# Kernel tuning notes

Hardware: AMD Instinct MI355X
Metric: run time of the kernel (lower is better)

The kernel has to match this reference:

```python
import jax, jax.numpy as jnp
import numpy as np

B, NH, N = 4, 4, 1000
NF = 256
TOPK = 10
ADJ_THRESH = 0.5
PSTEP = 3
BIG = 1e10


def construct_edges(s_cur, a_cur):
    """Top-k distance-based edge construction.
    s_cur: (B,N,3) positions, a_cur: (B,N) attributes; tool = a_cur > 0.5.
    Returns dense receiver/sender matrices Rr, Rs of shape (B, R=N*TOPK, N),
    padded with zero rows (equivalent to torch's contiguous packing).
    """
    b, n, _ = s_cur.shape
    tool = a_cur > 0.5  # mask is all-ones (no particle_nums)
    diff = s_cur[:, :, None, :] - s_cur[:, None, :, :]          # (B,N,N,3)
    dis = jnp.sum(diff * diff, axis=-1)                          # (B,N,N)
    # tool-tool pairs excluded (set huge distance)
    dis = jnp.where(tool[:, :, None] & tool[:, None, :], BIG, dis)
    neg_d, idx = jax.lax.top_k(-dis, TOPK)                       # smallest TOPK dists
    d = -neg_d                                                    # (B,N,TOPK)
    # edge valid if within threshold; receiver-is-tool edges zeroed
    # (connect_tools_all=False branch: adj[tool_mask_1 * mask_2] = 0)
    flag = (d < ADJ_THRESH * ADJ_THRESH) & (~tool[:, :, None])   # (B,N,TOPK)
    R = n * TOPK
    flagR = flag.reshape(b, R).astype(s_cur.dtype)
    send = idx.reshape(b, R)                                      # sender index per relation
    recv = jnp.repeat(jnp.arange(n), TOPK)                        # (R,) receiver index
    bi = jnp.arange(b)[:, None]
    ri = jnp.arange(R)[None, :]
    Rr = jnp.zeros((b, R, n), s_cur.dtype).at[bi, ri, recv[None, :]].set(flagR)
    Rs = jnp.zeros((b, R, n), s_cur.dtype).at[bi, ri, send].set(flagR)
    return Rr, Rs


def _forward(a_hist, s_hist, s_delta,
             pe_w0, pe_b0, pe_w1, pe_b1,
             re_w0, re_b0, re_w1, re_b1, re_w2, re_b2,
             rp_w, rp_b, pp_w, pp_b,
             pr_w0, pr_b0, pr_w1, pr_b1):
    relu = jax.nn.relu
    b, nh, n = a_hist.shape
    a = jnp.swapaxes(a_hist, 1, 2)                 # (B,N,NH)
    s = jnp.swapaxes(s_hist, 1, 2)                 # (B,N,NH,3)
    sd = jnp.swapaxes(s_delta, 1, 2).reshape(b, n, 3 * nh)  # (B,N,3*NH)
    a_cur = a[:, :, -1]                             # (B,N)
    s_cur = s[:, :, -1, :]                          # (B,N,3)

    Rr, Rs = construct_edges(s_cur, a_cur)          # (B,R,N)

    a_r = jnp.einsum('brn,bn->br', Rr, a_cur)[..., None]  # (B,R,1)
    a_s = jnp.einsum('brn,bn->br', Rs, a_cur)[..., None]
    s_r = jnp.einsum('brn,bnd->brd', Rr, s_cur)            # (B,R,3)
    s_s = jnp.einsum('brn,bnd->brd', Rs, s_cur)

    # particle encoder: Linear-ReLU-Linear-ReLU on cat[s_delta_flat, a_hist]
    pe_in = jnp.concatenate([sd, a], axis=2)               # (B,N,4*NH)
    particle_encode = relu(relu(pe_in @ pe_w0 + pe_b0) @ pe_w1 + pe_b1)

    re_in = jnp.concatenate([a_r, a_s, s_r - s_s], axis=2)
    h = relu(re_in @ re_w0 + re_b0)
    h = relu(h @ re_w1 + re_b1)
    relation_encode = relu(h @ re_w2 + re_b2)              # (B,R,NF)

    particle_effect = particle_encode
    for _ in range(PSTEP):
        eff_r = jnp.einsum('brn,bnd->brd', Rr, particle_effect)
        eff_s = jnp.einsum('brn,bnd->brd', Rs, particle_effect)
        effect_rel = relu(
            jnp.concatenate([relation_encode, eff_r, eff_s], axis=2) @ rp_w + rp_b)
        agg = jnp.einsum('brn,brd->bnd', Rr, effect_rel)   # Rr^T @ effect_rel
        particle_effect = relu(
            jnp.concatenate([particle_encode, agg], axis=2) @ pp_w + pp_b
            + particle_effect)

    pred = relu(particle_effect @ pr_w0 + pr_b0) @ pr_w1 + pr_b1  # (B,N,3)
    return pred + s_cur


def setup_inputs() -> dict:
    key = jax.random.key(0)
    ks = jax.random.split(key, 24)
    W = lambda k, shp: (jax.random.normal(k, shp, jnp.float32) * 0.05)
    inp = {
        'a_hist': jax.random.uniform(ks[0], (B, NH, N), jnp.float32),
        's_hist': jax.random.normal(ks[1], (B, NH, N, 3), jnp.float32),
        's_delta': jax.random.normal(ks[2], (B, NH, N, 3), jnp.float32),
        'pe_w0': W(ks[3], (4 * NH, NF)), 'pe_b0': W(ks[4], (NF,)),
        'pe_w1': W(ks[5], (NF, NF)),     'pe_b1': W(ks[6], (NF,)),
        're_w0': W(ks[7], (5, NF)),      're_b0': W(ks[8], (NF,)),
        're_w1': W(ks[9], (NF, NF)),     're_b1': W(ks[10], (NF,)),
        're_w2': W(ks[11], (NF, NF)),    're_b2': W(ks[12], (NF,)),
        'rp_w': W(ks[13], (3 * NF, NF)), 'rp_b': W(ks[14], (NF,)),
        'pp_w': W(ks[15], (2 * NF, NF)), 'pp_b': W(ks[16], (NF,)),
        'pr_w0': W(ks[17], (NF, NF)),    'pr_b0': W(ks[18], (NF,)),
        'pr_w1': W(ks[19], (NF, 3)),     'pr_b1': W(ks[20], (3,)),
    }
    return inp


def reference(a_hist, s_hist, s_delta,
              pe_w0, pe_b0, pe_w1, pe_b1,
              re_w0, re_b0, re_w1, re_b1, re_w2, re_b2,
              rp_w, rp_b, pp_w, pp_b,
              pr_w0, pr_b0, pr_w1, pr_b1):
    return _forward(a_hist, s_hist, s_delta,
                    pe_w0, pe_b0, pe_w1, pe_b1,
                    re_w0, re_b0, re_w1, re_b1, re_w2, re_b2,
                    rp_w, rp_b, pp_w, pp_b,
                    pr_w0, pr_b0, pr_w1, pr_b1)
```

## Files before the change

kernel.cpp:

```cpp
#include <hip/hip_runtime.h>
#include <hip/hip_bf16.h>

typedef unsigned short u16;
typedef unsigned int u32;

#define BATCH 4
#define NHIST 4
#define NPART 1000
#define NTOPK 10
#define NPT (BATCH*NPART)
#define NET (NPT*NTOPK)
#define EREG 5000
#define NRT 157

typedef __bf16 b8v __attribute__((ext_vector_type(8)));
typedef float  f4v __attribute__((ext_vector_type(4)));

__device__ __forceinline__ float bf2f(u16 b){
    return __uint_as_float(((u32)b) << 16);
}
__device__ __forceinline__ u16 f2bf(float f){
    u32 u = __float_as_uint(f);
    u32 r = u + 0x7FFF + ((u >> 16) & 1);
    return (u16)(r >> 16);
}
__device__ __forceinline__ float ldin(const void* p, size_t i, int isf32){
    return isf32 ? ((const float*)p)[i] : bf2f(((const u16*)p)[i]);
}
__device__ __forceinline__ void unp8(uint4 v, float* d){
    d[0]=bf2f((u16)v.x); d[1]=bf2f((u16)(v.x>>16));
    d[2]=bf2f((u16)v.y); d[3]=bf2f((u16)(v.y>>16));
    d[4]=bf2f((u16)v.z); d[5]=bf2f((u16)(v.z>>16));
    d[6]=bf2f((u16)v.w); d[7]=bf2f((u16)(v.w>>16));
}
__device__ __forceinline__ u32 pk2(float a, float b){
    return (u32)f2bf(a) | ((u32)f2bf(b) << 16);
}

__global__ __launch_bounds__(256) void k_setup(
    const void* __restrict__ a_hist, const void* __restrict__ s_hist,
    const void* __restrict__ s_delta,
    const void* w0, const void* w1, const void* w2, const void* w3,
    const void* w4, const void* w5, const void* w6, const void* w7,
    u16* __restrict__ wsw, int* __restrict__ dflag,
    float* __restrict__ s_cur, u16* __restrict__ pe_in,
    int* __restrict__ ecount8, int* __restrict__ cidx, int* __restrict__ csend,
    u16* __restrict__ re_in)
{
    __shared__ u32 SMEM[8192];
    __shared__ int sdet;
    __shared__ int wcnt[4], wbase[4];
    int t = threadIdx.x;
    if (t == 0) sdet = 0;
    __syncthreads();
    {
        const u16* p = (const u16*)a_hist;
        int bad = 0;
        for (int i = t; i < 2000; i += 256) bad |= (p[i] >> 15) & 1;
        if (bad) atomicOr(&sdet, 1);
    }
    __syncthreads();
    int isf32 = sdet;
    int bid = blockIdx.x;

    if (bid < 74){
        const int nck[8] = {1,8,1,8,8,24,16,8};
        const int Ks[8]  = {16,256,5,256,256,768,512,256};
        const void* srcs[8] = {w0,w1,w2,w3,w4,w5,w6,w7};
        int wi = 0, c = bid;
        while (c >= nck[wi]){ c -= nck[wi]; wi++; }
        const void* src = srcs[wi];
        int K = Ks[wi];
        u16* stage = (u16*)SMEM;
        #pragma unroll 4
        for (int kk = 0; kk < 32; kk++){
            int k = c*32 + kk;
            float v = (k < K) ? ldin(src, (size_t)k*256 + t, isf32) : 0.f;
            int e = (t >> 4)*512 + ((kk >> 3)*16 + (t & 15))*8 + (kk & 7);
            stage[e] = f2bf(v);
        }
        __syncthreads();
        uint4* dstv = (uint4*)(wsw + (size_t)bid * 8192);
        const uint4* sv = (const uint4*)stage;
        dstv[t] = sv[t];
        dstv[t + 256] = sv[t + 256];
        dstv[t + 512] = sv[t + 512];
        dstv[t + 768] = sv[t + 768];
        return;
    }
    if (bid < 90){
        if (bid == 74 && t == 0) dflag[0] = isf32;
        int g = (bid - 74)*256 + t;
        if (g >= NPT) return;
        int b = g / NPART, i = g - b*NPART;
        #pragma unroll
        for (int d = 0; d < 3; d++)
            s_cur[g*3 + d] = ldin(s_hist, (size_t)((b*NHIST + NHIST-1)*NPART + i)*3 + d, isf32);
        #pragma unroll
        for (int h = 0; h < NHIST; h++){
            #pragma unroll
            for (int d = 0; d < 3; d++)
                pe_in[g*32 + h*3 + d] = f2bf(ldin(s_delta, (size_t)((b*NHIST + h)*NPART + i)*3 + d, isf32));
            pe_in[g*32 + 12 + h] = f2bf(ldin(a_hist, (b*NHIST + h)*NPART + i, isf32));
        }
        #pragma unroll
        for (int k = 16; k < 32; k++) pe_in[g*32 + k] = 0;
        return;
    }
    float* sx = (float*)SMEM;
    float* sy = sx + 1000;
    float* sz = sx + 2000;
    float* sa = sx + 3000;
    u32* raw  = SMEM + 4096;
    u32* rawa = SMEM + 4096 + 3072;
    int tb = bid - 90;
    int b = tb / 250, r0 = (tb % 250) * 4;
    int wid = t >> 6, lane = t & 63;
    {
        int sbase = (b*NHIST + NHIST-1)*NPART*3;
        int abase = (b*NHIST + NHIST-1)*NPART;
        if (isf32){
            const uint4* ps = (const uint4*)((const float*)s_hist + sbase);
            for (int i = t; i < 750; i += 256) ((uint4*)raw)[i] = ps[i];
            const uint4* pa = (const uint4*)((const float*)a_hist + abase);
            if (t < 250) ((uint4*)rawa)[t] = pa[t];
        } else {
            const uint4* ps = (const uint4*)((const u16*)s_hist + sbase);
            for (int i = t; i < 375; i += 256) ((uint4*)raw)[i] = ps[i];
            const uint4* pa = (const uint4*)((const u16*)a_hist + abase);
            if (t < 125) ((uint4*)rawa)[t] = pa[t];
        }
    }
    __syncthreads();
    for (int j = t; j < NPART; j += 256){
        float vx, vy, vz, va;
        if (isf32){
            vx = ((const float*)raw)[j*3+0]; vy = ((const float*)raw)[j*3+1];
            vz = ((const float*)raw)[j*3+2]; va = ((const float*)rawa)[j];
        } else {
            vx = bf2f(((const u16*)raw)[j*3+0]); vy = bf2f(((const u16*)raw)[j*3+1]);
            vz = bf2f(((const u16*)raw)[j*3+2]); va = bf2f(((const u16*)rawa)[j]);
        }
        sx[j] = vx; sy[j] = vy; sz[j] = vz; sa[j] = va;
    }
    __syncthreads();
    int i = r0 + wid;
    float xi = sx[i], yi = sy[i], zi = sz[i];
    float ai = sa[i];
    bool tool_i = ai > 0.5f;
    float thr = tool_i ? -1.0f : 0.25f;

    float bd[NTOPK]; int bj[NTOPK];
    #pragma unroll
    for (int k = 0; k < NTOPK; k++){ bd[k] = 3.0e38f; bj[k] = 1 << 30; }
    for (int j = lane; j < NPART; j += 64){
        float dx = xi - sx[j], dy = yi - sy[j], dz = zi - sz[j];
        float d = dx*dx + dy*dy + dz*dz;
        if (d < thr && d < bd[NTOPK-1]){
            float v = d; int vj = j;
            #pragma unroll
            for (int k = 0; k < NTOPK; k++){
                bool sw = v < bd[k];
                float tv = bd[k]; int tj = bj[k];
                if (sw){ bd[k] = v; bj[k] = vj; v = tv; vj = tj; }
            }
        }
    }
    float myd = 3.0e38f; int myj = 0;
    #pragma unroll
    for (int r = 0; r < NTOPK; r++){
        float v = bd[0]; int vj = bj[0];
        #pragma unroll
        for (int s = 32; s > 0; s >>= 1){
            float ov = __shfl_xor(v, s);
            int   oj = __shfl_xor(vj, s);
            if (ov < v || (ov == v && oj < vj)){ v = ov; vj = oj; }
        }
        if (lane == r){ myd = v; myj = vj; }
        bool owner = (bd[0] == v) && (bj[0] == vj);
        if (owner){
            #pragma unroll
            for (int k = 0; k < NTOPK-1; k++){ bd[k] = bd[k+1]; bj[k] = bj[k+1]; }
            bd[NTOPK-1] = 3.0e38f; bj[NTOPK-1] = 1 << 30;
        }
    }
    bool fl = (lane < NTOPK) && (myd < 0.25f);
    int cnt = __popcll(__ballot(fl));
    if (lane == 0) wcnt[wid] = cnt;
    __syncthreads();
    if (t == 0){
        int c0 = wcnt[0], c1 = wcnt[1], c2 = wcnt[2], c3 = wcnt[3];
        int reg = tb & 7;
        int bb = atomicAdd(&ecount8[reg], c0 + c1 + c2 + c3) + reg*EREG;
        wbase[0] = bb; wbase[1] = bb + c0; wbase[2] = bb + c0 + c1; wbase[3] = bb + c0 + c1 + c2;
    }
    __syncthreads();
    int base = wbase[wid];
    if (lane < NTOPK){
        int gp = b*NPART + i;
        int ce = fl ? base + lane : -1;
        cidx[gp*NTOPK + lane] = ce;
        if (ce >= 0){
            int j = myj;
            csend[ce] = b*NPART + j;
            u32 q0 = (u32)f2bf(ai)        | ((u32)f2bf(sa[j])      << 16);
            u32 q1 = (u32)f2bf(xi - sx[j]) | ((u32)f2bf(yi - sy[j]) << 16);
            u32 q2 = (u32)f2bf(zi - sz[j]);
            uint4 v0 = {q0, q1, q2, 0};
            uint4 zz = {0, 0, 0, 0};
            uint4* rp = (uint4*)(re_in + (size_t)ce*32);
            rp[0] = v0; rp[1] = zz; rp[2] = zz; rp[3] = zz;
        }
    }
}

__global__ __launch_bounds__(256) void k_edge(
    const u16* __restrict__ re_in, const u16* __restrict__ pe_in,
    const u16* __restrict__ W0, const u16* __restrict__ W1,
    const u16* __restrict__ W2, const u16* __restrict__ W3,
    const u16* __restrict__ PW0, const u16* __restrict__ PW1,
    const u16* __restrict__ WrpB,
    const void* __restrict__ B0, const void* __restrict__ B1,
    const void* __restrict__ B2,
    const void* __restrict__ PB0, const void* __restrict__ PB1,
    const int* __restrict__ dflag, const int* __restrict__ ecount8,
    u16* __restrict__ Eout, u16* __restrict__ penc,
    u16* __restrict__ Pr, u16* __restrict__ Ps)
{
    __shared__ u16 H1[32*256];
    __shared__ u16 H2[32*256];
    __shared__ u16 S[32*32];
    int t = threadIdx.x, lane = t & 63, wave = t >> 6;
    int wm = wave >> 1, wn = wave & 1;
    int isf32 = dflag[0];
    int l15 = lane & 15, l4 = lane >> 4;

    f4v acc[8];
    b8v af, bfA[8], bfB[8];
    auto zacc = [&](){
        #pragma unroll
        for (int j = 0; j < 8; j++) acc[j] = {0.f,0.f,0.f,0.f};
    };
    auto rdWto = [&](b8v* dst, const u16* W, int kc){
        #pragma unroll
        for (int j = 0; j < 8; j++)
            dst[j] = *(const b8v*)(W + (size_t)kc*8192 + ((wn*8 + j)*64 + lane)*8);
    };
    auto domf = [&](b8v* wf){
        #pragma unroll
        for (int j = 0; j < 8; j++)
            acc[j] = __builtin_amdgcn_mfma_f32_16x16x32_bf16(af, wf[j], acc[j], 0, 0, 0);
    };
    auto rdA = [&](const u16* Hin, int kc){
        int R = wm*16 + l15;
        int up = (kc*4 + l4) ^ (R & 31);
        af = *(const b8v*)&Hin[R*256 + up*8];
    };
    auto layer = [&](const u16* Hin, const u16* Wg){
        zacc();
        rdWto(bfA, Wg, 0);
        #pragma unroll
        for (int kc = 0; kc < 8; kc += 2){
            rdWto(bfB, Wg, kc + 1);
            rdA(Hin, kc); domf(bfA);
            if (kc + 2 < 8) rdWto(bfA, Wg, kc + 2);
            rdA(Hin, kc + 1); domf(bfB);
        }
    };
    auto epiLDS = [&](u16* Hout, const void* Wb){
        #pragma unroll
        for (int j = 0; j < 8; j++){
            int col = (wn*8 + j)*16 + l15;
            float bias = ldin(Wb, col, isf32);
            int rb = wm*16 + l4*4;
            #pragma unroll
            for (int r = 0; r < 4; r++){
                float v = acc[j][r] + bias;
                v = v > 0.f ? v : 0.f;
                int rr = rb + r;
                int up = (col >> 3) ^ (rr & 31);
                Hout[rr*256 + up*8 + (col & 7)] = f2bf(v);
            }
        }
    };
    auto stLin = [&](u16* C, int row0){
        #pragma unroll
        for (int j = 0; j < 8; j++){
            int col = (wn*8 + j)*16 + l15;
            int rb = row0 + wm*16 + l4*4;
            #pragma unroll
            for (int r = 0; r < 4; r++)
                C[(size_t)(rb + r)*256 + col] = f2bf(acc[j][r]);
        }
    };

    if (blockIdx.x >= 8*NRT){
        int row0 = (blockIdx.x - 8*NRT) * 32;
        if (t < 128){
            int row = t >> 2, q = t & 3;
            int rg = row0 + row;
            uint4 v = *(const uint4*)(pe_in + (size_t)rg*32 + q*8);
            int up = q ^ (row & 3);
            *(uint4*)&S[row*32 + up*8] = v;
        }
        __syncthreads();
        zacc();
        {
            rdWto(bfA, PW0, 0);
            int R = wm*16 + l15;
            int up = l4 ^ (R & 3);
            af = *(const b8v*)&S[R*32 + up*8];
            domf(bfA);
        }
        epiLDS(H1, PB0);
        __syncthreads();
        layer(H1, PW1);
        #pragma unroll
        for (int j = 0; j < 8; j++){
            int col = (wn*8 + j)*16 + l15;
            float bias = ldin(PB1, col, isf32);
            int rb = wm*16 + l4*4;
            #pragma unroll
            for (int r = 0; r < 4; r++){
                int rr = rb + r;
                float v = acc[j][r] + bias;
                v = v > 0.f ? v : 0.f;
                penc[(size_t)(row0 + rr)*256 + col] = f2bf(v);
                int up = (col >> 3) ^ (rr & 31);
                H2[rr*256 + up*8 + (col & 7)] = f2bf(v);
            }
        }
        __syncthreads();
        layer(H2, WrpB);                      stLin(Pr, row0);
        layer(H2, WrpB + (size_t)8*8192);     stLin(Ps, row0);
        return;
    }

    int region = blockIdx.x / NRT;
    int local  = blockIdx.x - region*NRT;
    int ec = ecount8[region];
    if (local*32 >= ec) return;
    int row0 = region*EREG + local*32;
    if (t < 128){
        int row = t >> 2, q = t & 3;
        int rg = row0 + row; if (rg >= NET) rg = NET - 1;
        uint4 v = *(const uint4*)(re_in + (size_t)rg*32 + q*8);
        int up = q ^ (row & 3);
        *(uint4*)&S[row*32 + up*8] = v;
    }
    __syncthreads();

    zacc();
    {
        rdWto(bfA, W0, 0);
        int R = wm*16 + l15;
        int up = l4 ^ (R & 3);
        af = *(const b8v*)&S[R*32 + up*8];
        domf(bfA);
    }
    epiLDS(H1, B0);
    __syncthreads();
    layer(H1, W1); epiLDS(H2, B1);
    __syncthreads();
    layer(H2, W2); epiLDS(H1, B2);
    __syncthreads();
    layer(H1, W3);
    stLin(Eout, row0);
}

template<int MODE>
__global__ __launch_bounds__(256) void k_step(
    const u16* __restrict__ penc,
    const u16* __restrict__ Erel,
    const int* __restrict__ cidx, const int* __restrict__ csend,
    const u16* __restrict__ PrIn, const u16* __restrict__ PsIn,
    const void* __restrict__ rp_b,
    const u16* __restrict__ Wpp, const void* __restrict__ Bpp,
    const u16* __restrict__ res, u16* __restrict__ peff_out,
    const u16* __restrict__ WrpB, u16* __restrict__ PrOut, u16* __restrict__ PsOut,
    const u16* __restrict__ Wpr0, const void* __restrict__ Bpr0,
    const void* __restrict__ w1, const void* __restrict__ b1,
    const float* __restrict__ s_cur, void* __restrict__ out,
    const int* __restrict__ dflag)
{
    constexpr int SMW = (MODE == 1) ? (12288 + 4224 + 1536 + 8) : 12288;
    __shared__ u16 SM[SMW];
    u16* pencT = SM;
    u16* aggT  = SM + 4096;
    u16* H     = SM + 8192;
    int t = threadIdx.x, lane = t & 63, wn = t >> 6;
    int l15 = lane & 15, l4 = lane >> 4;
    int row0 = blockIdx.x * 16;
    int isf32 = dflag[0];

    {
        int row = t >> 4, cg = t & 15;
        int g = row0 + row;
        int c0 = cg * 16;
        int u0 = (cg*2) ^ row, u1 = (cg*2 + 1) ^ row;

        uint4 a0 = *(const uint4*)(penc + (size_t)g*256 + c0);
        uint4 a1 = *(const uint4*)(penc + (size_t)g*256 + c0 + 8);
        *(uint4*)&pencT[row*256 + u0*8] = a0;
        *(uint4*)&pencT[row*256 + u1*8] = a1;

        float prb[16];
        #pragma unroll
        for (int i = 0; i < 16; i++) prb[i] = ldin(rp_b, c0 + i, isf32);
        {
            uint4 p0 = *(const uint4*)(PrIn + (size_t)g*256 + c0);
            uint4 p1 = *(const uint4*)(PrIn + (size_t)g*256 + c0 + 8);
            float pv[16];
            unp8(p0, pv); unp8(p1, pv + 8);
            #pragma unroll
            for (int i = 0; i < 16; i++) prb[i] += pv[i];
        }
        float s[16];
        #pragma unroll
        for (int i = 0; i < 16; i++) s[i] = 0.f;
        #pragma unroll
        for (int k = 0; k < NTOPK; k++){
            int ce = cidx[g*NTOPK + k];
            if (ce >= 0){
                int sd = csend[ce];
                uint4 e0 = *(const uint4*)(Erel + (size_t)ce*256 + c0);
                uint4 e1 = *(const uint4*)(Erel + (size_t)ce*256 + c0 + 8);
                uint4 q0 = *(const uint4*)(PsIn + (size_t)sd*256 + c0);
                uint4 q1 = *(const uint4*)(PsIn + (size_t)sd*256 + c0 + 8);
                float ev[16], qv[16];
                unp8(e0, ev); unp8(e1, ev + 8);
                unp8(q0, qv); unp8(q1, qv + 8);
                #pragma unroll
                for (int i = 0; i < 16; i++){
                    float v = ev[i] + qv[i] + prb[i];
                    s[i] += v > 0.f ? v : 0.f;
                }
            }
        }
        uint4 z0, z1;
        z0.x = pk2(s[0],s[1]);   z0.y = pk2(s[2],s[3]);
        z0.z = pk2(s[4],s[5]);   z0.w = pk2(s[6],s[7]);
        z1.x = pk2(s[8],s[9]);   z1.y = pk2(s[10],s[11]);
        z1.z = pk2(s[12],s[13]); z1.w = pk2(s[14],s[15]);
        *(uint4*)&aggT[row*256 + u0*8] = z0;
        *(uint4*)&aggT[row*256 + u1*8] = z1;
    }

    f4v acc[4];
    b8v af, bfA[4], bfB[4];
    auto zacc = [&](){
        #pragma unroll
        for (int j = 0; j < 4; j++) acc[j] = {0.f,0.f,0.f,0.f};
    };
    auto rdWto = [&](b8v* dst, const u16* W, int kc){
        #pragma unroll
        for (int j = 0; j < 4; j++)
            dst[j] = *(const b8v*)(W + (size_t)kc*8192 + ((wn*4 + j)*64 + lane)*8);
    };
    auto domf = [&](b8v* wf){
        #pragma unroll
        for (int j = 0; j < 4; j++)
            acc[j] = __builtin_amdgcn_mfma_f32_16x16x32_bf16(af, wf[j], acc[j], 0, 0, 0);
    };
    auto rdH = [&](int kc){
        int R = l15;
        int up = (kc*4 + l4) ^ R;
        af = *(const b8v*)&H[R*256 + up*8];
    };
    auto rdA2 = [&](int kc){
        const u16* Hsrc = (kc < 8) ? pencT : aggT;
        int kk = kc & 7;
        int R = l15;
        int up = (kk*4 + l4) ^ R;
        af = *(const b8v*)&Hsrc[R*256 + up*8];
    };
    auto layer = [&](const u16* Wg){
        zacc();
        rdWto(bfA, Wg, 0);
        #pragma unroll
        for (int kc = 0; kc < 8; kc += 2){
            rdWto(bfB, Wg, kc + 1);
            rdH(kc); domf(bfA);
            if (kc + 2 < 8) rdWto(bfA, Wg, kc + 2);
            rdH(kc + 1); domf(bfB);
        }
    };
    auto stLin = [&](u16* C){
        #pragma unroll
        for (int j = 0; j < 4; j++){
            int col = (wn*4 + j)*16 + l15;
            int rb = row0 + l4*4;
            #pragma unroll
            for (int r = 0; r < 4; r++)
                C[(size_t)(rb + r)*256 + col] = f2bf(acc[j][r]);
        }
    };

    __syncthreads();

    zacc();
    rdWto(bfA, Wpp, 0);
    #pragma unroll
    for (int kc = 0; kc < 16; kc += 2){
        rdWto(bfB, Wpp, kc + 1);
        rdA2(kc); domf(bfA);
        if (kc + 2 < 16) rdWto(bfA, Wpp, kc + 2);
        rdA2(kc + 1); domf(bfB);
    }
    #pragma unroll
    for (int j = 0; j < 4; j++){
        int col = (wn*4 + j)*16 + l15;
        float bias = ldin(Bpp, col, isf32);
        int rb = l4*4;
        #pragma unroll
        for (int r = 0; r < 4; r++){
            int rr = rb + r;
            int row = row0 + rr;
            float v = acc[j][r] + bias + bf2f(res[(size_t)row*256 + col]);
            v = v > 0.f ? v : 0.f;
            int up = (col >> 3) ^ rr;
            H[rr*256 + up*8 + (col & 7)] = f2bf(v);
            if (MODE == 0) peff_out[(size_t)row*256 + col] = f2bf(v);
        }
    }
    __syncthreads();
    if (MODE == 0){
        layer(WrpB);                     stLin(PrOut);
        layer(WrpB + (size_t)8*8192);    stLin(PsOut);
    } else {
        u16* PH = SM + 12288;
        float* sw1 = (float*)(SM + 12288 + 4224);
        float* sb1 = (float*)(SM + 12288 + 4224 + 1536);
        #pragma unroll
        for (int i = 0; i < 3; i++) sw1[t + i*256] = ldin(w1, t + i*256, isf32);
        if (t < 3) sb1[t] = ldin(b1, t, isf32);
        layer(Wpr0);
        #pragma unroll
        for (int j = 0; j < 4; j++){
            int col = (wn*4 + j)*16 + l15;
            float bias = ldin(Bpr0, col, isf32);
            int rb = l4*4;
            #pragma unroll
            for (int r = 0; r < 4; r++){
                float v = acc[j][r] + bias;
                PH[(rb + r)*264 + col] = f2bf(v > 0.f ? v : 0.f);
            }
        }
        __syncthreads();
        int row = t >> 3, dd = t & 7;
        if (t < 128 && dd < 3){
            int g = row0 + row;
            float s = sb1[dd] + s_cur[g*3 + dd];
            const u16* hr = &PH[row*264];
            #pragma unroll 8
            for (int k = 0; k < 256; k++)
                s += bf2f(hr[k]) * sw1[k*3 + dd];
            if (isf32) ((float*)out)[g*3 + dd] = s;
            else       ((u16*)out)[g*3 + dd]   = f2bf(s);
        }
    }
}

extern "C" void kernel_launch(void* const* d_in, const int* in_sizes, int n_in,
                              void* d_out, int out_size, void* d_ws, size_t ws_size,
                              hipStream_t stream) {
    const void* a_hist = d_in[0];
    const void* s_hist = d_in[1];
    const void* s_delta= d_in[2];
    const void* pe_w0 = d_in[3];  const void* pe_b0 = d_in[4];
    const void* pe_w1 = d_in[5];  const void* pe_b1 = d_in[6];
    const void* re_w0 = d_in[7];  const void* re_b0 = d_in[8];
    const void* re_w1 = d_in[9];  const void* re_b1 = d_in[10];
    const void* re_w2 = d_in[11]; const void* re_b2 = d_in[12];
    const void* rp_w  = d_in[13]; const void* rp_b  = d_in[14];
    const void* pp_w  = d_in[15]; const void* pp_b  = d_in[16];
    const void* pr_w0 = d_in[17]; const void* pr_b0 = d_in[18];
    const void* pr_w1 = d_in[19]; const void* pr_b1 = d_in[20];

    char* base = (char*)d_ws;
    size_t off = 0;
    auto alloc = [&](size_t bytes) -> char* {
        char* p = base + off;
        off += (bytes + 255) & ~(size_t)255;
        return p;
    };
    int*   dflag = (int*)  alloc(16);
    int*   ecount8 = (int*)alloc(64);
    float* s_cur = (float*)alloc(NPT*3*4);
    int*   cidx  = (int*)  alloc(NET*4);
    int*   csend = (int*)  alloc(NET*4);
    u16* pe_in = (u16*)alloc((size_t)NPT*32*2);
    u16* re_in = (u16*)alloc((size_t)NET*32*2);
    u16* penc  = (u16*)alloc((size_t)NPT*256*2);
    u16* peffA = (u16*)alloc((size_t)NPT*256*2);
    u16* peffB = (u16*)alloc((size_t)NPT*256*2);
    u16* PrPs  = (u16*)alloc((size_t)4*NPT*256*2);
    u16* Erel  = (u16*)alloc((size_t)NET*256*2);
    u16* wsw   = (u16*)alloc((size_t)74*8192*2);

    u16* sw_pe0 = wsw + (size_t) 0*8192;
    u16* sw_pe1 = wsw + (size_t) 1*8192;
    u16* sw_re0 = wsw + (size_t) 9*8192;
    u16* sw_re1 = wsw + (size_t)10*8192;
    u16* sw_re2 = wsw + (size_t)18*8192;
    u16* sw_rp  = wsw + (size_t)26*8192;
    u16* sw_pp  = wsw + (size_t)50*8192;
    u16* sw_pr0 = wsw + (size_t)66*8192;

    u16* PrA = PrPs;
    u16* PsA = PrPs + (size_t)NPT*256;
    u16* PrB = PrPs + (size_t)2*NPT*256;
    u16* PsB = PrPs + (size_t)3*NPT*256;
    u16* sw_rpB = sw_rp + (size_t)8*8192;

    hipMemsetAsync(ecount8, 0, 32, stream);

    k_setup<<<1090, 256, 0, stream>>>(a_hist, s_hist, s_delta,
        pe_w0, pe_w1, re_w0, re_w1, re_w2, rp_w, pp_w, pr_w0,
        wsw, dflag, s_cur, pe_in, ecount8, cidx, csend, re_in);

    k_edge<<<8*NRT + 125, 256, 0, stream>>>(re_in, pe_in,
        sw_re0, sw_re1, sw_re2, sw_rp, sw_pe0, sw_pe1, sw_rpB,
        re_b0, re_b1, re_b2, pe_b0, pe_b1, dflag, ecount8, Erel, penc, PrA, PsA);

    k_step<0><<<250, 256, 0, stream>>>(penc, Erel, cidx, csend, PrA, PsA, rp_b,
        sw_pp, pp_b, penc, peffA, sw_rpB, PrB, PsB,
        nullptr, nullptr, nullptr, nullptr, nullptr, nullptr, dflag);
    k_step<0><<<250, 256, 0, stream>>>(penc, Erel, cidx, csend, PrB, PsB, rp_b,
        sw_pp, pp_b, peffA, peffB, sw_rpB, PrA, PsA,
        nullptr, nullptr, nullptr, nullptr, nullptr, nullptr, dflag);
    k_step<1><<<250, 256, 0, stream>>>(penc, Erel, cidx, csend, PrA, PsA, rp_b,
        sw_pp, pp_b, peffB, nullptr, nullptr, nullptr, nullptr,
        sw_pr0, pr_b0, pr_w1, pr_b1, s_cur, (void*)d_out, dflag);
}
```

Baseline: 218.6 us.

## Fuse three propagation steps into one cooperative kernel with grid sync

Replaces the three per-step k_step launches with a single cooperative kernel (250 blocks of 512 threads) that loops over the propagation steps and uses grid.sync between them. The particle effect and receiver projection stay in LDS across steps instead of round-tripping through global memory, and the edge indices and sender ids are loaded once into registers. Each wave now computes two output column tiles instead of four. This is meant to remove launch gaps and global traffic for intermediate tensors. In exchange it adds grid-wide barriers, uses more LDS per block, and relies on all 250 blocks being co-resident.

```diff
diff --git a/kernel.cpp b/kernel.cpp
--- a/kernel.cpp
+++ b/kernel.cpp
@@ -1,5 +1,6 @@
 #include <hip/hip_runtime.h>
 #include <hip/hip_bf16.h>
+#include <hip/hip_cooperative_groups.h>
 
 typedef unsigned short u16;
 typedef unsigned int u32;
@@ -368,111 +369,76 @@
     stLin(Eout, row0);
 }
 
-template<int MODE>
-__global__ __launch_bounds__(256) void k_step(
-    const u16* __restrict__ penc,
-    const u16* __restrict__ Erel,
+__global__ __launch_bounds__(512) void k_prop(
+    const u16* __restrict__ penc, const u16* __restrict__ Erel,
     const int* __restrict__ cidx, const int* __restrict__ csend,
-    const u16* __restrict__ PrIn, const u16* __restrict__ PsIn,
+    const u16* __restrict__ Pr0, u16* __restrict__ PsA, u16* __restrict__ PsB,
     const void* __restrict__ rp_b,
     const u16* __restrict__ Wpp, const void* __restrict__ Bpp,
-    const u16* __restrict__ res, u16* __restrict__ peff_out,
-    const u16* __restrict__ WrpB, u16* __restrict__ PrOut, u16* __restrict__ PsOut,
+    const u16* __restrict__ WrpB,
     const u16* __restrict__ Wpr0, const void* __restrict__ Bpr0,
     const void* __restrict__ w1, const void* __restrict__ b1,
     const float* __restrict__ s_cur, void* __restrict__ out,
     const int* __restrict__ dflag)
 {
-    constexpr int SMW = (MODE == 1) ? (12288 + 4224 + 1536 + 8) : 12288;
-    __shared__ u16 SM[SMW];
+    __shared__ u16 SM[22152];
     u16* pencT = SM;
     u16* aggT  = SM + 4096;
     u16* H     = SM + 8192;
-    int t = threadIdx.x, lane = t & 63, wn = t >> 6;
+    u16* PrL   = SM + 12288;
+    u16* PH    = SM + 16384;
+    float* sw1 = (float*)(SM + 20608);
+    float* sb1 = (float*)(SM + 22144);
+
+    cooperative_groups::grid_group grid = cooperative_groups::this_grid();
+
+    int t = threadIdx.x, lane = t & 63, wv = t >> 6;
     int l15 = lane & 15, l4 = lane >> 4;
     int row0 = blockIdx.x * 16;
     int isf32 = dflag[0];
 
+    int grow = t >> 5;
+    int cg = t & 31;
+    int c0g = cg * 8;
+    int g = row0 + grow;
     {
-        int row = t >> 4, cg = t & 15;
-        int g = row0 + row;
-        int c0 = cg * 16;
-        int u0 = (cg*2) ^ row, u1 = (cg*2 + 1) ^ row;
-
-        uint4 a0 = *(const uint4*)(penc + (size_t)g*256 + c0);
-        uint4 a1 = *(const uint4*)(penc + (size_t)g*256 + c0 + 8);
-        *(uint4*)&pencT[row*256 + u0*8] = a0;
-        *(uint4*)&pencT[row*256 + u1*8] = a1;
-
-        float prb[16];
-        #pragma unroll
-        for (int i = 0; i < 16; i++) prb[i] = ldin(rp_b, c0 + i, isf32);
-        {
-            uint4 p0 = *(const uint4*)(PrIn + (size_t)g*256 + c0);
-            uint4 p1 = *(const uint4*)(PrIn + (size_t)g*256 + c0 + 8);
-            float pv[16];
-            unp8(p0, pv); unp8(p1, pv + 8);
-            #pragma unroll
-            for (int i = 0; i < 16; i++) prb[i] += pv[i];
-        }
-        float s[16];
-        #pragma unroll
-        for (int i = 0; i < 16; i++) s[i] = 0.f;
-        #pragma unroll
-        for (int k = 0; k < NTOPK; k++){
-            int ce = cidx[g*NTOPK + k];
-            if (ce >= 0){
-                int sd = csend[ce];
-                uint4 e0 = *(const uint4*)(Erel + (size_t)ce*256 + c0);
-                uint4 e1 = *(const uint4*)(Erel + (size_t)ce*256 + c0 + 8);
-                uint4 q0 = *(const uint4*)(PsIn + (size_t)sd*256 + c0);
-                uint4 q1 = *(const uint4*)(PsIn + (size_t)sd*256 + c0 + 8);
-                float ev[16], qv[16];
-                unp8(e0, ev); unp8(e1, ev + 8);
-                unp8(q0, qv); unp8(q1, qv + 8);
-                #pragma unroll
-                for (int i = 0; i < 16; i++){
-                    float v = ev[i] + qv[i] + prb[i];
-                    s[i] += v > 0.f ? v : 0.f;
-                }
-            }
-        }
-        uint4 z0, z1;
-        z0.x = pk2(s[0],s[1]);   z0.y = pk2(s[2],s[3]);
-        z0.z = pk2(s[4],s[5]);   z0.w = pk2(s[6],s[7]);
-        z1.x = pk2(s[8],s[9]);   z1.y = pk2(s[10],s[11]);
-        z1.z = pk2(s[12],s[13]); z1.w = pk2(s[14],s[15]);
-        *(uint4*)&aggT[row*256 + u0*8] = z0;
-        *(uint4*)&aggT[row*256 + u1*8] = z1;
-    }
-
-    f4v acc[4];
-    b8v af, bfA[4], bfB[4];
+        uint4 pv = *(const uint4*)(penc + (size_t)g*256 + c0g);
+        *(uint4*)&pencT[grow*256 + (cg ^ grow)*8] = pv;
+    }
+    float rb8[8];
+    #pragma unroll
+    for (int i = 0; i < 8; i++) rb8[i] = ldin(rp_b, c0g + i, isf32);
+    int cel[NTOPK], sdl[NTOPK];
+    #pragma unroll
+    for (int k = 0; k < NTOPK; k++){
+        cel[k] = cidx[g*NTOPK + k];
+        sdl[k] = (cel[k] >= 0) ? csend[cel[k]] : 0;
+    }
+
+    f4v acc[2];
+    b8v af, bfA[2], bfB[2];
     auto zacc = [&](){
-        #pragma unroll
-        for (int j = 0; j < 4; j++) acc[j] = {0.f,0.f,0.f,0.f};
+        acc[0] = {0.f,0.f,0.f,0.f}; acc[1] = {0.f,0.f,0.f,0.f};
     };
     auto rdWto = [&](b8v* dst, const u16* W, int kc){
         #pragma unroll
-        for (int j = 0; j < 4; j++)
-            dst[j] = *(const b8v*)(W + (size_t)kc*8192 + ((wn*4 + j)*64 + lane)*8);
+        for (int j = 0; j < 2; j++)
+            dst[j] = *(const b8v*)(W + (size_t)kc*8192 + ((wv*2 + j)*64 + lane)*8);
     };
     auto domf = [&](b8v* wf){
         #pragma unroll
-        for (int j = 0; j < 4; j++)
+        for (int j = 0; j < 2; j++)
             acc[j] = __builtin_amdgcn_mfma_f32_16x16x32_bf16(af, wf[j], acc[j], 0, 0, 0);
     };
     auto rdH = [&](int kc){
-        int R = l15;
-        int up = (kc*4 + l4) ^ R;
-        af = *(const b8v*)&H[R*256 + up*8];
+        int up = (kc*4 + l4) ^ l15;
+        af = *(const b8v*)&H[l15*256 + up*8];
     };
     auto rdA2 = [&](int kc){
-        const u16* Hsrc = (kc < 8) ? pencT : aggT;
+        const u16* Hs = (kc < 8) ? pencT : aggT;
         int kk = kc & 7;
-        int R = l15;
-        int up = (kk*4 + l4) ^ R;
-        af = *(const b8v*)&Hsrc[R*256 + up*8];
+        int up = (kk*4 + l4) ^ l15;
+        af = *(const b8v*)&Hs[l15*256 + up*8];
     };
     auto layer = [&](const u16* Wg){
         zacc();
@@ -485,78 +451,114 @@
             rdH(kc + 1); domf(bfB);
         }
     };
-    auto stLin = [&](u16* C){
-        #pragma unroll
-        for (int j = 0; j < 4; j++){
-            int col = (wn*4 + j)*16 + l15;
-            int rb = row0 + l4*4;
-            #pragma unroll
-            for (int r = 0; r < 4; r++)
-                C[(size_t)(rb + r)*256 + col] = f2bf(acc[j][r]);
-        }
-    };
-
-    __syncthreads();
-
-    zacc();
-    rdWto(bfA, Wpp, 0);
-    #pragma unroll
-    for (int kc = 0; kc < 16; kc += 2){
-        rdWto(bfB, Wpp, kc + 1);
-        rdA2(kc); domf(bfA);
-        if (kc + 2 < 16) rdWto(bfA, Wpp, kc + 2);
-        rdA2(kc + 1); domf(bfB);
-    }
-    #pragma unroll
-    for (int j = 0; j < 4; j++){
-        int col = (wn*4 + j)*16 + l15;
-        float bias = ldin(Bpp, col, isf32);
-        int rb = l4*4;
-        #pragma unroll
-        for (int r = 0; r < 4; r++){
-            int rr = rb + r;
-            int row = row0 + rr;
-            float v = acc[j][r] + bias + bf2f(res[(size_t)row*256 + col]);
-            v = v > 0.f ? v : 0.f;
-            int up = (col >> 3) ^ rr;
-            H[rr*256 + up*8 + (col & 7)] = f2bf(v);
-            if (MODE == 0) peff_out[(size_t)row*256 + col] = f2bf(v);
-        }
-    }
-    __syncthreads();
-    if (MODE == 0){
-        layer(WrpB);                     stLin(PrOut);
-        layer(WrpB + (size_t)8*8192);    stLin(PsOut);
-    } else {
-        u16* PH = SM + 12288;
-        float* sw1 = (float*)(SM + 12288 + 4224);
-        float* sb1 = (float*)(SM + 12288 + 4224 + 1536);
-        #pragma unroll
-        for (int i = 0; i < 3; i++) sw1[t + i*256] = ldin(w1, t + i*256, isf32);
-        if (t < 3) sb1[t] = ldin(b1, t, isf32);
-        layer(Wpr0);
-        #pragma unroll
-        for (int j = 0; j < 4; j++){
-            int col = (wn*4 + j)*16 + l15;
-            float bias = ldin(Bpr0, col, isf32);
-            int rb = l4*4;
+
+    for (int s = 0; s < 3; s++){
+        {
+            const u16* PsIn = (s == 1) ? PsB : PsA;
+            float prv[8];
+            if (s == 0){
+                uint4 p0 = *(const uint4*)(Pr0 + (size_t)g*256 + c0g);
+                unp8(p0, prv);
+            } else {
+                #pragma unroll
+                for (int i = 0; i < 8; i++) prv[i] = bf2f(PrL[grow*256 + c0g + i]);
+            }
+            #pragma unroll
+            for (int i = 0; i < 8; i++) prv[i] += rb8[i];
+            float sa[8];
+            #pragma unroll
+            for (int i = 0; i < 8; i++) sa[i] = 0.f;
+            #pragma unroll
+            for (int k = 0; k < NTOPK; k++){
+                if (cel[k] >= 0){
+                    uint4 e0 = *(const uint4*)(Erel + (size_t)cel[k]*256 + c0g);
+                    uint4 q0 = *(const uint4*)(PsIn + (size_t)sdl[k]*256 + c0g);
+                    float ev[8], qv[8];
+                    unp8(e0, ev); unp8(q0, qv);
+                    #pragma unroll
+                    for (int i = 0; i < 8; i++){
+                        float v = ev[i] + qv[i] + prv[i];
+                        sa[i] += v > 0.f ? v : 0.f;
+                    }
+                }
+            }
+            uint4 z;
+            z.x = pk2(sa[0],sa[1]); z.y = pk2(sa[2],sa[3]);
+            z.z = pk2(sa[4],sa[5]); z.w = pk2(sa[6],sa[7]);
+            *(uint4*)&aggT[grow*256 + (cg ^ grow)*8] = z;
+        }
+        __syncthreads();
+
+        zacc();
+        rdWto(bfA, Wpp, 0);
+        #pragma unroll
+        for (int kc = 0; kc < 16; kc += 2){
+            rdWto(bfB, Wpp, kc + 1);
+            rdA2(kc); domf(bfA);
+            if (kc + 2 < 16) rdWto(bfA, Wpp, kc + 2);
+            rdA2(kc + 1); domf(bfB);
+        }
+        #pragma unroll
+        for (int j = 0; j < 2; j++){
+            int col = (wv*2 + j)*16 + l15;
+            float bias = ldin(Bpp, col, isf32);
             #pragma unroll
             for (int r = 0; r < 4; r++){
-                float v = acc[j][r] + bias;
-                PH[(rb + r)*264 + col] = f2bf(v > 0.f ? v : 0.f);
+                int rr = l4*4 + r;
+                int e = rr*256 + ((col >> 3) ^ rr)*8 + (col & 7);
+                float resv = bf2f((s == 0) ? pencT[e] : H[e]);
+                float v = acc[j][r] + bias + resv;
+                v = v > 0.f ? v : 0.f;
+                H[e] = f2bf(v);
             }
         }
         __syncthreads();
-        int row = t >> 3, dd = t & 7;
-        if (t < 128 && dd < 3){
-            int g = row0 + row;
-            float s = sb1[dd] + s_cur[g*3 + dd];
-            const u16* hr = &PH[row*264];
-            #pragma unroll 8
-            for (int k = 0; k < 256; k++)
-                s += bf2f(hr[k]) * sw1[k*3 + dd];
-            if (isf32) ((float*)out)[g*3 + dd] = s;
-            else       ((u16*)out)[g*3 + dd]   = f2bf(s);
+
+        if (s < 2){
+            u16* PsOut = (s == 0) ? PsB : PsA;
+            layer(WrpB);
+            #pragma unroll
+            for (int j = 0; j < 2; j++){
+                int col = (wv*2 + j)*16 + l15;
+                #pragma unroll
+                for (int r = 0; r < 4; r++)
+                    PrL[(l4*4 + r)*256 + col] = f2bf(acc[j][r]);
+            }
+            layer(WrpB + (size_t)8*8192);
+            #pragma unroll
+            for (int j = 0; j < 2; j++){
+                int col = (wv*2 + j)*16 + l15;
+                #pragma unroll
+                for (int r = 0; r < 4; r++)
+                    PsOut[(size_t)(row0 + l4*4 + r)*256 + col] = f2bf(acc[j][r]);
+            }
+            grid.sync();
+        } else {
+            for (int i = t; i < 768; i += 512) sw1[i] = ldin(w1, i, isf32);
+            if (t < 3) sb1[t] = ldin(b1, t, isf32);
+            layer(Wpr0);
+            #pragma unroll
+            for (int j = 0; j < 2; j++){
+                int col = (wv*2 + j)*16 + l15;
+                float bias = ldin(Bpr0, col, isf32);
+                #pragma unroll
+                for (int r = 0; r < 4; r++){
+                    float v = acc[j][r] + bias;
+                    PH[(l4*4 + r)*264 + col] = f2bf(v > 0.f ? v : 0.f);
+                }
+            }
+            __syncthreads();
+            int row = t >> 3, dd = t & 7;
+            if (t < 128 && dd < 3){
+                int gg = row0 + row;
+                float sv = sb1[dd] + s_cur[gg*3 + dd];
+                const u16* hr = &PH[row*264];
+                #pragma unroll 8
+                for (int k = 0; k < 256; k++)
+                    sv += bf2f(hr[k]) * sw1[k*3 + dd];
+                if (isf32) ((float*)out)[gg*3 + dd] = sv;
+                else       ((u16*)out)[gg*3 + dd]   = f2bf(sv);
+            }
         }
     }
 }
@@ -592,9 +594,9 @@
     u16* pe_in = (u16*)alloc((size_t)NPT*32*2);
     u16* re_in = (u16*)alloc((size_t)NET*32*2);
     u16* penc  = (u16*)alloc((size_t)NPT*256*2);
-    u16* peffA = (u16*)alloc((size_t)NPT*256*2);
-    u16* peffB = (u16*)alloc((size_t)NPT*256*2);
-    u16* PrPs  = (u16*)alloc((size_t)4*NPT*256*2);
+    u16* Pr0   = (u16*)alloc((size_t)NPT*256*2);
+    u16* PsA   = (u16*)alloc((size_t)NPT*256*2);
+    u16* PsB   = (u16*)alloc((size_t)NPT*256*2);
     u16* Erel  = (u16*)alloc((size_t)NET*256*2);
     u16* wsw   = (u16*)alloc((size_t)74*8192*2);
 
@@ -606,11 +608,6 @@
     u16* sw_rp  = wsw + (size_t)26*8192;
     u16* sw_pp  = wsw + (size_t)50*8192;
     u16* sw_pr0 = wsw + (size_t)66*8192;
-
-    u16* PrA = PrPs;
-    u16* PsA = PrPs + (size_t)NPT*256;
-    u16* PrB = PrPs + (size_t)2*NPT*256;
-    u16* PsB = PrPs + (size_t)3*NPT*256;
     u16* sw_rpB = sw_rp + (size_t)8*8192;
 
     hipMemsetAsync(ecount8, 0, 32, stream);
@@ -621,15 +618,22 @@
 
     k_edge<<<8*NRT + 125, 256, 0, stream>>>(re_in, pe_in,
         sw_re0, sw_re1, sw_re2, sw_rp, sw_pe0, sw_pe1, sw_rpB,
-        re_b0, re_b1, re_b2, pe_b0, pe_b1, dflag, ecount8, Erel, penc, PrA, PsA);
-
-    k_step<0><<<250, 256, 0, stream>>>(penc, Erel, cidx, csend, PrA, PsA, rp_b,
-        sw_pp, pp_b, penc, peffA, sw_rpB, PrB, PsB,
-        nullptr, nullptr, nullptr, nullptr, nullptr, nullptr, dflag);
-    k_step<0><<<250, 256, 0, stream>>>(penc, Erel, cidx, csend, PrB, PsB, rp_b,
-        sw_pp, pp_b, peffA, peffB, sw_rpB, PrA, PsA,
-        nullptr, nullptr, nullptr, nullptr, nullptr, nullptr, dflag);
-    k_step<1><<<250, 256, 0, stream>>>(penc, Erel, cidx, csend, PrA, PsA, rp_b,
-        sw_pp, pp_b, peffB, nullptr, nullptr, nullptr, nullptr,
-        sw_pr0, pr_b0, pr_w1, pr_b1, s_cur, (void*)d_out, dflag);
-}
+        re_b0, re_b1, re_b2, pe_b0, pe_b1, dflag, ecount8, Erel, penc, Pr0, PsA);
+
+    {
+        const u16* a_penc = penc;  const u16* a_Erel = Erel;
+        const int* a_cidx = cidx;  const int* a_csend = csend;
+        const u16* a_Pr0 = Pr0;    u16* a_PsA = PsA;  u16* a_PsB = PsB;
+        const void* a_rpb = rp_b;
+        const u16* a_Wpp = sw_pp;  const void* a_Bpp = pp_b;
+        const u16* a_WrpB = sw_rpB;
+        const u16* a_Wpr0 = sw_pr0; const void* a_Bpr0 = pr_b0;
+        const void* a_w1 = pr_w1;  const void* a_b1 = pr_b1;
+        const float* a_scur = s_cur; void* a_out = d_out;
+        const int* a_dflag = dflag;
+        void* args[] = {&a_penc, &a_Erel, &a_cidx, &a_csend, &a_Pr0, &a_PsA, &a_PsB,
+                        &a_rpb, &a_Wpp, &a_Bpp, &a_WrpB, &a_Wpr0, &a_Bpr0,
+                        &a_w1, &a_b1, &a_scur, &a_out, &a_dflag};
+        hipLaunchCooperativeKernel((void*)k_prop, dim3(250), dim3(512), args, 0, stream);
+    }
+}
```

New measurement: 329.7 us. 1.51x slower.
